# Kernel tuning notes

Hardware: AMD Instinct MI355X
Metric: run time of the kernel (lower is better)

## Reference

```python
import jax, jax.numpy as jnp
import numpy as np

NPOINT = 1024
RADIUS = 0.2
NSAMPLE = 32


def fps(xyz, npoint):
    """Furthest point sampling. xyz: (B, N, 3) -> idx (B, npoint) int32.
    Sequential farthest-distance selection, first point is index 0 (matches CUDA kernel)."""
    def one(pts):
        N = pts.shape[0]
        def step(carry, _):
            dists, last = carry
            d = jnp.sum((pts - pts[last]) ** 2, axis=-1)   # (N,)
            dists = jnp.minimum(dists, d)
            nxt = jnp.argmax(dists).astype(jnp.int32)
            return (dists, nxt), last
        init = (jnp.full((N,), 1e10, dtype=pts.dtype), jnp.int32(0))
        _, idx = jax.lax.scan(step, init, None, length=npoint)
        return idx
    return jax.vmap(one)(xyz)


def ball_query(xyz, new_xyz, radius, nsample):
    """For each centroid, indices of first nsample points within radius;
    slots with no hit are filled with the first hit (centroid itself is always a hit)."""
    N = xyz.shape[1]
    d2 = jnp.sum((new_xyz[:, :, None, :] - xyz[:, None, :, :]) ** 2, axis=-1)  # (B, npoint, N)
    cand = jnp.where(d2 < radius * radius, jnp.arange(N, dtype=jnp.int32), jnp.int32(N))
    neg_topk, _ = jax.lax.top_k(-cand, nsample)  # smallest nsample candidate indices
    idx = -neg_topk                               # ascending order, misses == N
    first = idx[..., :1]
    return jnp.where(idx == N, first, idx)


_batched_gather = jax.vmap(lambda a, i: a[i])  # a: (N, C), i: (...,) -> (..., C)


def reference(xyz, normal, features, w1, b1, w2, b2, w3, b3):
    # --- FPS sampling + gather of centroids ---
    fps_idx = fps(xyz, NPOINT)                          # (B, npoint)
    new_xyz = _batched_gather(xyz, fps_idx)             # (B, npoint, 3)
    new_normal = _batched_gather(normal, fps_idx)       # (B, npoint, 3)

    # --- ball-query grouping ---
    idx = ball_query(xyz, new_xyz, RADIUS, NSAMPLE)     # (B, npoint, nsample)
    grouped_xyz = _batched_gather(xyz, idx) - new_xyz[:, :, None, :]  # relative coords
    grouped_feat = _batched_gather(features, idx)        # (B, npoint, nsample, C)
    h = jnp.concatenate([grouped_xyz, grouped_feat], axis=-1)  # (B, npoint, nsample, 3+C)

    # --- shared per-neighborhood MLP (1x1 convs) + max pool over neighbors ---
    h = jax.nn.relu(jnp.einsum('bpsc,co->bpso', h, w1) + b1)
    h = jax.nn.relu(jnp.einsum('bpsc,co->bpso', h, w2) + b2)
    h = jax.nn.relu(jnp.einsum('bpsc,co->bpso', h, w3) + b3)
    new_features = jnp.max(h, axis=2)                   # (B, npoint, 128)
    new_features = jnp.transpose(new_features, (0, 2, 1))  # (B, 128, npoint) channel-first
    return new_xyz, new_normal, new_features


def setup_inputs() -> dict:
    key = jax.random.key(0)
    ks = jax.random.split(key, 9)
    B, N, C = 8, 8192, 32
    cin = 3 + C
    return {
        'xyz': jax.random.uniform(ks[0], (B, N, 3), dtype=jnp.float32),
        'normal': jax.random.normal(ks[1], (B, N, 3), dtype=jnp.float32),
        'features': jax.random.normal(ks[2], (B, N, C), dtype=jnp.float32),
        'w1': jax.random.normal(ks[3], (cin, 64), dtype=jnp.float32) * (1.0 / np.sqrt(cin)),
        'b1': jnp.zeros((64,), dtype=jnp.float32),
        'w2': jax.random.normal(ks[4], (64, 64), dtype=jnp.float32) * (1.0 / np.sqrt(64)),
        'b2': jnp.zeros((64,), dtype=jnp.float32),
        'w3': jax.random.normal(ks[5], (64, 128), dtype=jnp.float32) * (1.0 / np.sqrt(64)),
        'b3': jnp.zeros((128,), dtype=jnp.float32),
    }
```

## Files before the change

### kernel.cpp

```cpp
#include <hip/hip_runtime.h>

#define NB 8
#define NN 8192
#define NC 32
#define NPOINT 1024
#define NSAMPLE 32

__device__ __forceinline__ float d2_exact(float ax, float ay, float az,
                                          float bx, float by, float bz) {
    float dx = __fsub_rn(ax, bx);
    float dy = __fsub_rn(ay, by);
    float dz = __fsub_rn(az, bz);
    return __fadd_rn(__fadd_rn(__fmul_rn(dx, dx), __fmul_rn(dy, dy)),
                     __fmul_rn(dz, dz));
}

#define FPS_T 256
#define FPS_K (NN / FPS_T)

__device__ __forceinline__ unsigned long long kmax64(unsigned long long a,
                                                     unsigned long long b) {
    return a > b ? a : b;
}

template <int CTRL, int RM>
__device__ __forceinline__ unsigned long long dpp_k(unsigned long long k) {
    unsigned hi = (unsigned)__builtin_amdgcn_update_dpp(
        0, (int)(k >> 32), CTRL, RM, 0xf, true);
    unsigned lo = (unsigned)__builtin_amdgcn_update_dpp(
        0, (int)(k & 0xffffffffULL), CTRL, RM, 0xf, true);
    return ((unsigned long long)hi << 32) | lo;
}

__global__ __launch_bounds__(FPS_T, 1) void fps_kernel(
    const float* __restrict__ xyz, const float* __restrict__ normal,
    float* __restrict__ out_xyz, float* __restrict__ out_normal) {
    const int b = blockIdx.x;
    const float* bx = xyz + (size_t)b * NN * 3;
    const int tid = threadIdx.x;
    const int lane = tid & 63;
    const int wave = tid >> 6;

    __shared__ unsigned long long redk[2][4];
    __shared__ int sel_hist[NPOINT];

    float px[FPS_K], py[FPS_K], pz[FPS_K], dist[FPS_K];
#pragma unroll
    for (int k = 0; k < FPS_K; ++k) {
        int p = tid + k * FPS_T;
        px[k] = bx[p * 3 + 0];
        py[k] = bx[p * 3 + 1];
        pz[k] = bx[p * 3 + 2];
        dist[k] = 1e10f;
    }
#pragma unroll
    for (int k = 0; k < FPS_K; ++k) {
        asm volatile("" : "+v"(px[k]), "+v"(py[k]), "+v"(pz[k]));
    }

    int cur = 0;
    float lx = bx[0], ly = bx[1], lz = bx[2];

    for (int it = 0; it < NPOINT; ++it) {
        const int par = it & 1;
        if (tid == 0) sel_hist[it] = cur;

        float bv = -1.0f;
        int bk = 0;
#pragma unroll
        for (int k = 0; k < FPS_K; ++k) {
            float d = d2_exact(px[k], py[k], pz[k], lx, ly, lz);
            float nd = fminf(dist[k], d);
            dist[k] = nd;
            bool gt = nd > bv;
            bv = gt ? nd : bv;
            bk = gt ? k : bk;
        }
        int bp = tid + (bk << 8);
        unsigned long long key =
            ((unsigned long long)__float_as_uint(bv) << 32) |
            (unsigned)(~bp);

        key = kmax64(key, dpp_k<0x111, 0xf>(key));
        key = kmax64(key, dpp_k<0x112, 0xf>(key));
        key = kmax64(key, dpp_k<0x114, 0xf>(key));
        key = kmax64(key, dpp_k<0x118, 0xf>(key));
        key = kmax64(key, dpp_k<0x142, 0xa>(key));
        key = kmax64(key, dpp_k<0x143, 0xc>(key));
        if (lane == 63) redk[par][wave] = key;
        __syncthreads();

        unsigned long long g =
            kmax64(kmax64(redk[par][0], redk[par][1]),
                   kmax64(redk[par][2], redk[par][3]));
        int p = (int)(~(unsigned)(g & 0xffffffffULL));
        p = __builtin_amdgcn_readfirstlane(p);
        const float* lp = bx + 3 * (size_t)p;
        lx = lp[0]; ly = lp[1]; lz = lp[2];
        cur = p;
    }
    __syncthreads();

    const float* bn = normal + (size_t)b * NN * 3;
    for (int t = tid; t < NPOINT; t += FPS_T) {
        int i = sel_hist[t];
        size_t o = ((size_t)b * NPOINT + t) * 3;
        out_xyz[o + 0] = bx[i * 3 + 0];
        out_xyz[o + 1] = bx[i * 3 + 1];
        out_xyz[o + 2] = bx[i * 3 + 2];
        out_normal[o + 0] = bn[i * 3 + 0];
        out_normal[o + 1] = bn[i * 3 + 1];
        out_normal[o + 2] = bn[i * 3 + 2];
    }
}

#define K2_WAVES 2
#define XS 37
#define HS 65

__global__ __launch_bounds__(64 * K2_WAVES) void group_mlp_kernel(
    const float* __restrict__ xyz, const float* __restrict__ features,
    const float* __restrict__ w1, const float* __restrict__ b1,
    const float* __restrict__ w2, const float* __restrict__ b2,
    const float* __restrict__ w3, const float* __restrict__ b3,
    const float* __restrict__ new_xyz, float* __restrict__ out_feat) {
    const int wave = threadIdx.x >> 6;
    const int lane = threadIdx.x & 63;
    const int g = blockIdx.x * K2_WAVES + wave;
    const int b = g >> 10;
    const int p = g & 1023;
    const float* bxp = xyz + (size_t)b * NN * 3;
    const float* bfp = features + (size_t)b * NN * NC;

    __shared__ int sel_s[K2_WAVES][NSAMPLE];
    __shared__ float bufA[K2_WAVES][32 * HS];
    __shared__ float bufB[K2_WAVES][32 * HS];

    const float cx = new_xyz[(size_t)g * 3 + 0];
    const float cy = new_xyz[(size_t)g * 3 + 1];
    const float cz = new_xyz[(size_t)g * 3 + 2];

    int have = 0;
    for (int ch = 0; ch < NN / 64 && have < NSAMPLE; ++ch) {
        int j = ch * 64 + lane;
        float x = bxp[j * 3 + 0], y = bxp[j * 3 + 1], z = bxp[j * 3 + 2];
        float d2 = d2_exact(x, y, z, cx, cy, cz);
        bool hit = d2 < 0.04f;
        unsigned long long m = __ballot(hit);
        int pos = have + __popcll(m & ((1ull << lane) - 1ull));
        if (hit && pos < NSAMPLE) sel_s[wave][pos] = j;
        have += __popcll(m);
    }
    __syncthreads();
    int nsel = have < NSAMPLE ? have : NSAMPLE;
    int first = sel_s[wave][0];
    if (lane < NSAMPLE && lane >= nsel) sel_s[wave][lane] = first;
    __syncthreads();

    {
        int s = lane >> 1, h = lane & 1;
        int row = sel_s[wave][s];
        float* X = &bufA[wave][0];
        const float* fr = bfp + (size_t)row * NC + h * 16;
#pragma unroll
        for (int q = 0; q < 4; ++q) {
            float4 v = *(const float4*)(fr + q * 4);
            int base = s * XS + 3 + h * 16 + q * 4;
            X[base + 0] = v.x; X[base + 1] = v.y;
            X[base + 2] = v.z; X[base + 3] = v.w;
        }
        if (h == 0) {
            X[s * XS + 0] = __fsub_rn(bxp[row * 3 + 0], cx);
            X[s * XS + 1] = __fsub_rn(bxp[row * 3 + 1], cy);
            X[s * XS + 2] = __fsub_rn(bxp[row * 3 + 2], cz);
        }
    }
    __syncthreads();

    const int sg = lane >> 3;
    const int og = lane & 7;

    {
        float acc[4][8];
#pragma unroll
        for (int j = 0; j < 4; ++j)
#pragma unroll
            for (int o = 0; o < 8; ++o) acc[j][o] = 0.f;
        const float* X = &bufA[wave][0];
        for (int c = 0; c < 35; ++c) {
            float xv[4];
#pragma unroll
            for (int j = 0; j < 4; ++j) xv[j] = X[(sg * 4 + j) * XS + c];
            const float* wr = w1 + c * 64 + og * 8;
            float4 wa = *(const float4*)(wr);
            float4 wb = *(const float4*)(wr + 4);
            float w8[8] = {wa.x, wa.y, wa.z, wa.w, wb.x, wb.y, wb.z, wb.w};
#pragma unroll
            for (int j = 0; j < 4; ++j)
#pragma unroll
                for (int o = 0; o < 8; ++o) acc[j][o] += xv[j] * w8[o];
        }
        float4 ba = *(const float4*)(b1 + og * 8);
        float4 bb = *(const float4*)(b1 + og * 8 + 4);
        float bias[8] = {ba.x, ba.y, ba.z, ba.w, bb.x, bb.y, bb.z, bb.w};
        float* H = &bufB[wave][0];
#pragma unroll
        for (int j = 0; j < 4; ++j)
#pragma unroll
            for (int o = 0; o < 8; ++o)
                H[(sg * 4 + j) * HS + og * 8 + o] = fmaxf(acc[j][o] + bias[o], 0.f);
    }
    __syncthreads();

    {
        float acc[4][8];
#pragma unroll
        for (int j = 0; j < 4; ++j)
#pragma unroll
            for (int o = 0; o < 8; ++o) acc[j][o] = 0.f;
        const float* H = &bufB[wave][0];
        for (int c = 0; c < 64; ++c) {
            float xv[4];
#pragma unroll
            for (int j = 0; j < 4; ++j) xv[j] = H[(sg * 4 + j) * HS + c];
            const float* wr = w2 + c * 64 + og * 8;
            float4 wa = *(const float4*)(wr);
            float4 wb = *(const float4*)(wr + 4);
            float w8[8] = {wa.x, wa.y, wa.z, wa.w, wb.x, wb.y, wb.z, wb.w};
#pragma unroll
            for (int j = 0; j < 4; ++j)
#pragma unroll
                for (int o = 0; o < 8; ++o) acc[j][o] += xv[j] * w8[o];
        }
        float4 ba = *(const float4*)(b2 + og * 8);
        float4 bb = *(const float4*)(b2 + og * 8 + 4);
        float bias[8] = {ba.x, ba.y, ba.z, ba.w, bb.x, bb.y, bb.z, bb.w};
        float* H2 = &bufA[wave][0];
#pragma unroll
        for (int j = 0; j < 4; ++j)
#pragma unroll
            for (int o = 0; o < 8; ++o)
                H2[(sg * 4 + j) * HS + og * 8 + o] = fmaxf(acc[j][o] + bias[o], 0.f);
    }
    __syncthreads();

    {
        float acc[4][16];
#pragma unroll
        for (int j = 0; j < 4; ++j)
#pragma unroll
            for (int o = 0; o < 16; ++o) acc[j][o] = 0.f;
        const float* H = &bufA[wave][0];
        for (int c = 0; c < 64; ++c) {
            float xv[4];
#pragma unroll
            for (int j = 0; j < 4; ++j) xv[j] = H[(sg * 4 + j) * HS + c];
            const float* wr = w3 + c * 128 + og * 16;
            float4 wq[4];
#pragma unroll
            for (int q = 0; q < 4; ++q) wq[q] = *(const float4*)(wr + q * 4);
            float w16[16] = {wq[0].x, wq[0].y, wq[0].z, wq[0].w,
                             wq[1].x, wq[1].y, wq[1].z, wq[1].w,
                             wq[2].x, wq[2].y, wq[2].z, wq[2].w,
                             wq[3].x, wq[3].y, wq[3].z, wq[3].w};
#pragma unroll
            for (int j = 0; j < 4; ++j)
#pragma unroll
                for (int o = 0; o < 16; ++o) acc[j][o] += xv[j] * w16[o];
        }
        float m[16];
#pragma unroll
        for (int o = 0; o < 16; ++o) {
            float t0 = fmaxf(acc[0][o], acc[1][o]);
            float t1 = fmaxf(acc[2][o], acc[3][o]);
            m[o] = fmaxf(t0, t1);
        }
#pragma unroll
        for (int off = 8; off <= 32; off <<= 1)
#pragma unroll
            for (int o = 0; o < 16; ++o) m[o] = fmaxf(m[o], __shfl_xor(m[o], off));
        if (sg == 0) {
            float4 bq[4];
#pragma unroll
            for (int q = 0; q < 4; ++q) bq[q] = *(const float4*)(b3 + og * 16 + q * 4);
            float bias[16] = {bq[0].x, bq[0].y, bq[0].z, bq[0].w,
                              bq[1].x, bq[1].y, bq[1].z, bq[1].w,
                              bq[2].x, bq[2].y, bq[2].z, bq[2].w,
                              bq[3].x, bq[3].y, bq[3].z, bq[3].w};
#pragma unroll
            for (int o = 0; o < 16; ++o) {
                float v = fmaxf(m[o] + bias[o], 0.f);
                out_feat[((size_t)b * 128 + og * 16 + o) * NPOINT + p] = v;
            }
        }
    }
}

extern "C" void kernel_launch(void* const* d_in, const int* in_sizes, int n_in,
                              void* d_out, int out_size, void* d_ws, size_t ws_size,
                              hipStream_t stream) {
    const float* xyz      = (const float*)d_in[0];
    const float* normal   = (const float*)d_in[1];
    const float* features = (const float*)d_in[2];
    const float* w1 = (const float*)d_in[3];
    const float* b1 = (const float*)d_in[4];
    const float* w2 = (const float*)d_in[5];
    const float* b2 = (const float*)d_in[6];
    const float* w3 = (const float*)d_in[7];
    const float* b3 = (const float*)d_in[8];

    float* out        = (float*)d_out;
    float* out_xyz    = out;
    float* out_normal = out + NB * NPOINT * 3;
    float* out_feat   = out + 2 * NB * NPOINT * 3;

    hipLaunchKernelGGL(fps_kernel, dim3(NB), dim3(FPS_T), 0, stream,
                       xyz, normal, out_xyz, out_normal);
    hipLaunchKernelGGL(group_mlp_kernel, dim3(NB * NPOINT / K2_WAVES),
                       dim3(64 * K2_WAVES), 0, stream,
                       xyz, features, w1, b1, w2, b2, w3, b3, out_xyz, out_feat);
}
```

Measured before the change: 1.184 ms.

## Widen FPS block to 512 threads, use packed FP32 math and LDS-staged coordinates

Doubles the FPS block to 512 threads (eight waves) so each thread holds half as many points. The distance computation now uses packed v_pk_add/v_pk_mul pairs. The selected point's coordinates are read from a 96KB LDS copy of the cloud instead of global memory, both per iteration and in the final gather. This shortens the serial per-iteration latency of the 1024-step loop, at the cost of a wider cross-wave reduction, more waves per barrier and heavy LDS use.

```diff
diff --git a/kernel.cpp b/kernel.cpp
--- a/kernel.cpp
+++ b/kernel.cpp
@@ -15,8 +15,22 @@
                      __fmul_rn(dz, dz));
 }
 
-#define FPS_T 256
+#define FPS_T 512
 #define FPS_K (NN / FPS_T)
+#define FPS_W (FPS_T / 64)
+
+typedef float f32x2 __attribute__((ext_vector_type(2)));
+
+__device__ __forceinline__ f32x2 pk_add(f32x2 a, f32x2 b) {
+    f32x2 d;
+    asm("v_pk_add_f32 %0, %1, %2" : "=v"(d) : "v"(a), "v"(b));
+    return d;
+}
+__device__ __forceinline__ f32x2 pk_mul(f32x2 a, f32x2 b) {
+    f32x2 d;
+    asm("v_pk_mul_f32 %0, %1, %2" : "=v"(d) : "v"(a), "v"(b));
+    return d;
+}
 
 __device__ __forceinline__ unsigned long long kmax64(unsigned long long a,
                                                      unsigned long long b) {
@@ -41,21 +55,28 @@
     const int lane = tid & 63;
     const int wave = tid >> 6;
 
-    __shared__ unsigned long long redk[2][4];
+    __shared__ float sxyz[NN * 3];
+    __shared__ unsigned long long redk[2][FPS_W];
     __shared__ int sel_hist[NPOINT];
 
-    float px[FPS_K], py[FPS_K], pz[FPS_K], dist[FPS_K];
+    f32x2 px[FPS_K / 2], py[FPS_K / 2], pz[FPS_K / 2];
+    float dist[FPS_K];
 #pragma unroll
     for (int k = 0; k < FPS_K; ++k) {
         int p = tid + k * FPS_T;
-        px[k] = bx[p * 3 + 0];
-        py[k] = bx[p * 3 + 1];
-        pz[k] = bx[p * 3 + 2];
+        float x = bx[p * 3 + 0];
+        float y = bx[p * 3 + 1];
+        float z = bx[p * 3 + 2];
+        sxyz[p * 3 + 0] = x;
+        sxyz[p * 3 + 1] = y;
+        sxyz[p * 3 + 2] = z;
+        if ((k & 1) == 0) { px[k >> 1].x = x; py[k >> 1].x = y; pz[k >> 1].x = z; }
+        else              { px[k >> 1].y = x; py[k >> 1].y = y; pz[k >> 1].y = z; }
         dist[k] = 1e10f;
     }
 #pragma unroll
-    for (int k = 0; k < FPS_K; ++k) {
-        asm volatile("" : "+v"(px[k]), "+v"(py[k]), "+v"(pz[k]));
+    for (int q = 0; q < FPS_K / 2; ++q) {
+        asm volatile("" : "+v"(px[q]), "+v"(py[q]), "+v"(pz[q]));
     }
 
     int cur = 0;
@@ -65,18 +86,31 @@
         const int par = it & 1;
         if (tid == 0) sel_hist[it] = cur;
 
+        f32x2 nlx = {-lx, -lx};
+        f32x2 nly = {-ly, -ly};
+        f32x2 nlz = {-lz, -lz};
+
         float bv = -1.0f;
         int bk = 0;
 #pragma unroll
-        for (int k = 0; k < FPS_K; ++k) {
-            float d = d2_exact(px[k], py[k], pz[k], lx, ly, lz);
-            float nd = fminf(dist[k], d);
-            dist[k] = nd;
-            bool gt = nd > bv;
-            bv = gt ? nd : bv;
-            bk = gt ? k : bk;
-        }
-        int bp = tid + (bk << 8);
+        for (int q = 0; q < FPS_K / 2; ++q) {
+            f32x2 dx = pk_add(px[q], nlx);
+            f32x2 dy = pk_add(py[q], nly);
+            f32x2 dz = pk_add(pz[q], nlz);
+            f32x2 d2 = pk_add(pk_add(pk_mul(dx, dx), pk_mul(dy, dy)),
+                              pk_mul(dz, dz));
+            float nd0 = fminf(dist[2 * q + 0], d2.x);
+            float nd1 = fminf(dist[2 * q + 1], d2.y);
+            dist[2 * q + 0] = nd0;
+            dist[2 * q + 1] = nd1;
+            bool g0 = nd0 > bv;
+            bv = g0 ? nd0 : bv;
+            bk = g0 ? 2 * q + 0 : bk;
+            bool g1 = nd1 > bv;
+            bv = g1 ? nd1 : bv;
+            bk = g1 ? 2 * q + 1 : bk;
+        }
+        int bp = tid + (bk << 9);
         unsigned long long key =
             ((unsigned long long)__float_as_uint(bv) << 32) |
             (unsigned)(~bp);
@@ -91,12 +125,15 @@
         __syncthreads();
 
         unsigned long long g =
-            kmax64(kmax64(redk[par][0], redk[par][1]),
-                   kmax64(redk[par][2], redk[par][3]));
+            kmax64(kmax64(kmax64(redk[par][0], redk[par][1]),
+                          kmax64(redk[par][2], redk[par][3])),
+                   kmax64(kmax64(redk[par][4], redk[par][5]),
+                          kmax64(redk[par][6], redk[par][7])));
         int p = (int)(~(unsigned)(g & 0xffffffffULL));
         p = __builtin_amdgcn_readfirstlane(p);
-        const float* lp = bx + 3 * (size_t)p;
-        lx = lp[0]; ly = lp[1]; lz = lp[2];
+        lx = sxyz[p * 3 + 0];
+        ly = sxyz[p * 3 + 1];
+        lz = sxyz[p * 3 + 2];
         cur = p;
     }
     __syncthreads();
@@ -105,9 +142,9 @@
     for (int t = tid; t < NPOINT; t += FPS_T) {
         int i = sel_hist[t];
         size_t o = ((size_t)b * NPOINT + t) * 3;
-        out_xyz[o + 0] = bx[i * 3 + 0];
-        out_xyz[o + 1] = bx[i * 3 + 1];
-        out_xyz[o + 2] = bx[i * 3 + 2];
+        out_xyz[o + 0] = sxyz[i * 3 + 0];
+        out_xyz[o + 1] = sxyz[i * 3 + 1];
+        out_xyz[o + 2] = sxyz[i * 3 + 2];
         out_normal[o + 0] = bn[i * 3 + 0];
         out_normal[o + 1] = bn[i * 3 + 1];
         out_normal[o + 2] = bn[i * 3 + 2];
```

After: 1.334 ms. +12.6%, slower.

## Fuse FPS and grouping MLP into one persistent kernel streaming centroid indices

Applied to the files above, without the earlier changes.

Merges the FPS and group/MLP kernels into a single cooperative persistent launch. 8 blocks run FPS and publish selected indices to a workspace in chunks of 16 via atomic stores. 248 consumer blocks spin-wait on those indices and run ball query plus the MLP as soon as each centroid is ready, so the grouping work overlaps the long sequential FPS. This adds polling overhead and relies on all blocks being co-resident, with a fallback to a normal launch if the cooperative launch fails.

```diff
diff --git a/kernel.cpp b/kernel.cpp
--- a/kernel.cpp
+++ b/kernel.cpp
@@ -17,6 +17,16 @@
 
 #define FPS_T 256
 #define FPS_K (NN / FPS_T)
+#define NCONS 248
+#define NBLK (NB + NCONS)
+#define K2_WAVES 4
+#define SLOTS_PER_PASS (NCONS * K2_WAVES)
+#define NPASS ((NB * NPOINT + SLOTS_PER_PASS - 1) / SLOTS_PER_PASS)
+
+#define XS 37
+#define HS 65
+
+#define SMEM_BYTES 90112
 
 __device__ __forceinline__ unsigned long long kmax64(unsigned long long a,
                                                      unsigned long long b) {
@@ -32,268 +42,294 @@
     return ((unsigned long long)hi << 32) | lo;
 }
 
-__global__ __launch_bounds__(FPS_T, 1) void fps_kernel(
+__global__ __launch_bounds__(256, 1) void fused_kernel(
     const float* __restrict__ xyz, const float* __restrict__ normal,
-    float* __restrict__ out_xyz, float* __restrict__ out_normal) {
-    const int b = blockIdx.x;
-    const float* bx = xyz + (size_t)b * NN * 3;
-    const int tid = threadIdx.x;
-    const int lane = tid & 63;
-    const int wave = tid >> 6;
-
-    __shared__ unsigned long long redk[2][4];
-    __shared__ int sel_hist[NPOINT];
-
-    float px[FPS_K], py[FPS_K], pz[FPS_K], dist[FPS_K];
-#pragma unroll
-    for (int k = 0; k < FPS_K; ++k) {
-        int p = tid + k * FPS_T;
-        px[k] = bx[p * 3 + 0];
-        py[k] = bx[p * 3 + 1];
-        pz[k] = bx[p * 3 + 2];
-        dist[k] = 1e10f;
-    }
-#pragma unroll
-    for (int k = 0; k < FPS_K; ++k) {
-        asm volatile("" : "+v"(px[k]), "+v"(py[k]), "+v"(pz[k]));
-    }
-
-    int cur = 0;
-    float lx = bx[0], ly = bx[1], lz = bx[2];
-
-    for (int it = 0; it < NPOINT; ++it) {
-        const int par = it & 1;
-        if (tid == 0) sel_hist[it] = cur;
-
-        float bv = -1.0f;
-        int bk = 0;
-#pragma unroll
-        for (int k = 0; k < FPS_K; ++k) {
-            float d = d2_exact(px[k], py[k], pz[k], lx, ly, lz);
-            float nd = fminf(dist[k], d);
-            dist[k] = nd;
-            bool gt = nd > bv;
-            bv = gt ? nd : bv;
-            bk = gt ? k : bk;
-        }
-        int bp = tid + (bk << 8);
-        unsigned long long key =
-            ((unsigned long long)__float_as_uint(bv) << 32) |
-            (unsigned)(~bp);
-
-        key = kmax64(key, dpp_k<0x111, 0xf>(key));
-        key = kmax64(key, dpp_k<0x112, 0xf>(key));
-        key = kmax64(key, dpp_k<0x114, 0xf>(key));
-        key = kmax64(key, dpp_k<0x118, 0xf>(key));
-        key = kmax64(key, dpp_k<0x142, 0xa>(key));
-        key = kmax64(key, dpp_k<0x143, 0xc>(key));
-        if (lane == 63) redk[par][wave] = key;
-        __syncthreads();
-
-        unsigned long long g =
-            kmax64(kmax64(redk[par][0], redk[par][1]),
-                   kmax64(redk[par][2], redk[par][3]));
-        int p = (int)(~(unsigned)(g & 0xffffffffULL));
-        p = __builtin_amdgcn_readfirstlane(p);
-        const float* lp = bx + 3 * (size_t)p;
-        lx = lp[0]; ly = lp[1]; lz = lp[2];
-        cur = p;
-    }
-    __syncthreads();
-
-    const float* bn = normal + (size_t)b * NN * 3;
-    for (int t = tid; t < NPOINT; t += FPS_T) {
-        int i = sel_hist[t];
-        size_t o = ((size_t)b * NPOINT + t) * 3;
-        out_xyz[o + 0] = bx[i * 3 + 0];
-        out_xyz[o + 1] = bx[i * 3 + 1];
-        out_xyz[o + 2] = bx[i * 3 + 2];
-        out_normal[o + 0] = bn[i * 3 + 0];
-        out_normal[o + 1] = bn[i * 3 + 1];
-        out_normal[o + 2] = bn[i * 3 + 2];
-    }
-}
-
-#define K2_WAVES 2
-#define XS 37
-#define HS 65
-
-__global__ __launch_bounds__(64 * K2_WAVES) void group_mlp_kernel(
-    const float* __restrict__ xyz, const float* __restrict__ features,
+    const float* __restrict__ features,
     const float* __restrict__ w1, const float* __restrict__ b1,
     const float* __restrict__ w2, const float* __restrict__ b2,
     const float* __restrict__ w3, const float* __restrict__ b3,
-    const float* __restrict__ new_xyz, float* __restrict__ out_feat) {
-    const int wave = threadIdx.x >> 6;
-    const int lane = threadIdx.x & 63;
-    const int g = blockIdx.x * K2_WAVES + wave;
-    const int b = g >> 10;
-    const int p = g & 1023;
-    const float* bxp = xyz + (size_t)b * NN * 3;
-    const float* bfp = features + (size_t)b * NN * NC;
-
-    __shared__ int sel_s[K2_WAVES][NSAMPLE];
-    __shared__ float bufA[K2_WAVES][32 * HS];
-    __shared__ float bufB[K2_WAVES][32 * HS];
-
-    const float cx = new_xyz[(size_t)g * 3 + 0];
-    const float cy = new_xyz[(size_t)g * 3 + 1];
-    const float cz = new_xyz[(size_t)g * 3 + 2];
-
-    int have = 0;
-    for (int ch = 0; ch < NN / 64 && have < NSAMPLE; ++ch) {
-        int j = ch * 64 + lane;
-        float x = bxp[j * 3 + 0], y = bxp[j * 3 + 1], z = bxp[j * 3 + 2];
-        float d2 = d2_exact(x, y, z, cx, cy, cz);
-        bool hit = d2 < 0.04f;
-        unsigned long long m = __ballot(hit);
-        int pos = have + __popcll(m & ((1ull << lane) - 1ull));
-        if (hit && pos < NSAMPLE) sel_s[wave][pos] = j;
-        have += __popcll(m);
+    float* __restrict__ out_xyz, float* __restrict__ out_normal,
+    float* __restrict__ out_feat, int* __restrict__ idxbuf) {
+
+    __shared__ __align__(16) char smem[SMEM_BYTES];
+
+    if (blockIdx.x < NB) {
+        unsigned long long (*redk)[4] = (unsigned long long (*)[4])(smem);
+        int* sel_hist = (int*)(smem + 64);
+
+        const int b = blockIdx.x;
+        const float* bx = xyz + (size_t)b * NN * 3;
+        const int tid = threadIdx.x;
+        const int lane = tid & 63;
+        const int wave = tid >> 6;
+        int* idxg = idxbuf + (b << 10);
+
+        float px[FPS_K], py[FPS_K], pz[FPS_K], dist[FPS_K];
+#pragma unroll
+        for (int k = 0; k < FPS_K; ++k) {
+            int p = tid + k * FPS_T;
+            px[k] = bx[p * 3 + 0];
+            py[k] = bx[p * 3 + 1];
+            pz[k] = bx[p * 3 + 2];
+            dist[k] = 1e10f;
+        }
+#pragma unroll
+        for (int k = 0; k < FPS_K; ++k) {
+            asm volatile("" : "+v"(px[k]), "+v"(py[k]), "+v"(pz[k]));
+        }
+
+        int cur = 0;
+        float lx = bx[0], ly = bx[1], lz = bx[2];
+
+        for (int it = 0; it < NPOINT; ++it) {
+            const int par = it & 1;
+            if (tid == 0) sel_hist[it] = cur;
+
+            float bv = -1.0f;
+            int bk = 0;
+#pragma unroll
+            for (int k = 0; k < FPS_K; ++k) {
+                float d = d2_exact(px[k], py[k], pz[k], lx, ly, lz);
+                float nd = fminf(dist[k], d);
+                dist[k] = nd;
+                bool gt = nd > bv;
+                bv = gt ? nd : bv;
+                bk = gt ? k : bk;
+            }
+            int bp = tid + (bk << 8);
+            unsigned long long key =
+                ((unsigned long long)__float_as_uint(bv) << 32) |
+                (unsigned)(~bp);
+
+            key = kmax64(key, dpp_k<0x111, 0xf>(key));
+            key = kmax64(key, dpp_k<0x112, 0xf>(key));
+            key = kmax64(key, dpp_k<0x114, 0xf>(key));
+            key = kmax64(key, dpp_k<0x118, 0xf>(key));
+            key = kmax64(key, dpp_k<0x142, 0xa>(key));
+            key = kmax64(key, dpp_k<0x143, 0xc>(key));
+            if (lane == 63) redk[par][wave] = key;
+            __syncthreads();
+
+            unsigned long long g =
+                kmax64(kmax64(redk[par][0], redk[par][1]),
+                       kmax64(redk[par][2], redk[par][3]));
+            int p = (int)(~(unsigned)(g & 0xffffffffULL));
+            p = __builtin_amdgcn_readfirstlane(p);
+            const float* lp = bx + 3 * (size_t)p;
+            lx = lp[0]; ly = lp[1]; lz = lp[2];
+            cur = p;
+
+            if (((it & 15) == 15) && tid < 16) {
+                int t = (it & ~15) + tid;
+                __hip_atomic_store(idxg + t, sel_hist[t], __ATOMIC_RELAXED,
+                                   __HIP_MEMORY_SCOPE_AGENT);
+            }
+        }
+        __syncthreads();
+
+        const float* bn = normal + (size_t)b * NN * 3;
+        for (int t = tid; t < NPOINT; t += FPS_T) {
+            int i = sel_hist[t];
+            size_t o = ((size_t)b * NPOINT + t) * 3;
+            out_xyz[o + 0] = bx[i * 3 + 0];
+            out_xyz[o + 1] = bx[i * 3 + 1];
+            out_xyz[o + 2] = bx[i * 3 + 2];
+            out_normal[o + 0] = bn[i * 3 + 0];
+            out_normal[o + 1] = bn[i * 3 + 1];
+            out_normal[o + 2] = bn[i * 3 + 2];
+        }
+    } else {
+        int*   sel_all  = (int*)smem;
+        float* bufA_all = (float*)(smem + 512);
+        float* bufB_all = (float*)(smem + 33792);
+
+        const int cb = blockIdx.x - NB;
+        const int wave = threadIdx.x >> 6;
+        const int lane = threadIdx.x & 63;
+        int*   sel = sel_all + wave * 32;
+        float* XA  = bufA_all + wave * 2080;
+        float* XB  = bufB_all + wave * 2080;
+
+        for (int pass = 0; pass < NPASS; ++pass) {
+            int k = pass * SLOTS_PER_PASS + (cb * K2_WAVES + wave);
+            if (k >= NB * NPOINT) k -= NB * NPOINT;
+            const int b = k & 7;
+            const int t = k >> 3;
+            const int g = (b << 10) + t;
+            const int p = t;
+            const float* bxp = xyz + (size_t)b * NN * 3;
+            const float* bfp = features + (size_t)b * NN * NC;
+
+            int v = __hip_atomic_load(idxbuf + g, __ATOMIC_RELAXED,
+                                      __HIP_MEMORY_SCOPE_AGENT);
+            while (v < 0) {
+                __builtin_amdgcn_s_sleep(8);
+                v = __hip_atomic_load(idxbuf + g, __ATOMIC_RELAXED,
+                                      __HIP_MEMORY_SCOPE_AGENT);
+            }
+            const float cx = bxp[v * 3 + 0];
+            const float cy = bxp[v * 3 + 1];
+            const float cz = bxp[v * 3 + 2];
+
+            int have = 0;
+            for (int ch = 0; ch < NN / 64 && have < NSAMPLE; ++ch) {
+                int j = ch * 64 + lane;
+                float x = bxp[j * 3 + 0], y = bxp[j * 3 + 1], z = bxp[j * 3 + 2];
+                float d2 = d2_exact(x, y, z, cx, cy, cz);
+                bool hit = d2 < 0.04f;
+                unsigned long long m = __ballot(hit);
+                int pos = have + __popcll(m & ((1ull << lane) - 1ull));
+                if (hit && pos < NSAMPLE) sel[pos] = j;
+                have += __popcll(m);
+            }
+            __syncthreads();
+            int nsel = have < NSAMPLE ? have : NSAMPLE;
+            int first = sel[0];
+            if (lane < NSAMPLE && lane >= nsel) sel[lane] = first;
+            __syncthreads();
+
+            {
+                int s = lane >> 1, h = lane & 1;
+                int row = sel[s];
+                const float* fr = bfp + (size_t)row * NC + h * 16;
+#pragma unroll
+                for (int q = 0; q < 4; ++q) {
+                    float4 vv = *(const float4*)(fr + q * 4);
+                    int base = s * XS + 3 + h * 16 + q * 4;
+                    XA[base + 0] = vv.x; XA[base + 1] = vv.y;
+                    XA[base + 2] = vv.z; XA[base + 3] = vv.w;
+                }
+                if (h == 0) {
+                    XA[s * XS + 0] = __fsub_rn(bxp[row * 3 + 0], cx);
+                    XA[s * XS + 1] = __fsub_rn(bxp[row * 3 + 1], cy);
+                    XA[s * XS + 2] = __fsub_rn(bxp[row * 3 + 2], cz);
+                }
+            }
+            __syncthreads();
+
+            const int sg = lane >> 3;
+            const int og = lane & 7;
+
+            {
+                float acc[4][8];
+#pragma unroll
+                for (int j = 0; j < 4; ++j)
+#pragma unroll
+                    for (int o = 0; o < 8; ++o) acc[j][o] = 0.f;
+                for (int c = 0; c < 35; ++c) {
+                    float xv[4];
+#pragma unroll
+                    for (int j = 0; j < 4; ++j) xv[j] = XA[(sg * 4 + j) * XS + c];
+                    const float* wr = w1 + c * 64 + og * 8;
+                    float4 wa = *(const float4*)(wr);
+                    float4 wb = *(const float4*)(wr + 4);
+                    float w8[8] = {wa.x, wa.y, wa.z, wa.w, wb.x, wb.y, wb.z, wb.w};
+#pragma unroll
+                    for (int j = 0; j < 4; ++j)
+#pragma unroll
+                        for (int o = 0; o < 8; ++o) acc[j][o] += xv[j] * w8[o];
+                }
+                float4 ba = *(const float4*)(b1 + og * 8);
+                float4 bb = *(const float4*)(b1 + og * 8 + 4);
+                float bias[8] = {ba.x, ba.y, ba.z, ba.w, bb.x, bb.y, bb.z, bb.w};
+#pragma unroll
+                for (int j = 0; j < 4; ++j)
+#pragma unroll
+                    for (int o = 0; o < 8; ++o)
+                        XB[(sg * 4 + j) * HS + og * 8 + o] =
+                            fmaxf(acc[j][o] + bias[o], 0.f);
+            }
+            __syncthreads();
+
+            {
+                float acc[4][8];
+#pragma unroll
+                for (int j = 0; j < 4; ++j)
+#pragma unroll
+                    for (int o = 0; o < 8; ++o) acc[j][o] = 0.f;
+                for (int c = 0; c < 64; ++c) {
+                    float xv[4];
+#pragma unroll
+                    for (int j = 0; j < 4; ++j) xv[j] = XB[(sg * 4 + j) * HS + c];
+                    const float* wr = w2 + c * 64 + og * 8;
+                    float4 wa = *(const float4*)(wr);
+                    float4 wb = *(const float4*)(wr + 4);
+                    float w8[8] = {wa.x, wa.y, wa.z, wa.w, wb.x, wb.y, wb.z, wb.w};
+#pragma unroll
+                    for (int j = 0; j < 4; ++j)
+#pragma unroll
+                        for (int o = 0; o < 8; ++o) acc[j][o] += xv[j] * w8[o];
+                }
+                float4 ba = *(const float4*)(b2 + og * 8);
+                float4 bb = *(const float4*)(b2 + og * 8 + 4);
+                float bias[8] = {ba.x, ba.y, ba.z, ba.w, bb.x, bb.y, bb.z, bb.w};
+#pragma unroll
+                for (int j = 0; j < 4; ++j)
+#pragma unroll
+                    for (int o = 0; o < 8; ++o)
+                        XA[(sg * 4 + j) * HS + og * 8 + o] =
+                            fmaxf(acc[j][o] + bias[o], 0.f);
+            }
+            __syncthreads();
+
+            {
+                float acc[4][16];
+#pragma unroll
+                for (int j = 0; j < 4; ++j)
+#pragma unroll
+                    for (int o = 0; o < 16; ++o) acc[j][o] = 0.f;
+                for (int c = 0; c < 64; ++c) {
+                    float xv[4];
+#pragma unroll
+                    for (int j = 0; j < 4; ++j) xv[j] = XA[(sg * 4 + j) * HS + c];
+                    const float* wr = w3 + c * 128 + og * 16;
+                    float4 wq[4];
+#pragma unroll
+                    for (int q = 0; q < 4; ++q) wq[q] = *(const float4*)(wr + q * 4);
+                    float w16[16] = {wq[0].x, wq[0].y, wq[0].z, wq[0].w,
+                                     wq[1].x, wq[1].y, wq[1].z, wq[1].w,
+                                     wq[2].x, wq[2].y, wq[2].z, wq[2].w,
+                                     wq[3].x, wq[3].y, wq[3].z, wq[3].w};
+#pragma unroll
+                    for (int j = 0; j < 4; ++j)
+#pragma unroll
+                        for (int o = 0; o < 16; ++o) acc[j][o] += xv[j] * w16[o];
+                }
+                float m[16];
+#pragma unroll
+                for (int o = 0; o < 16; ++o) {
+                    float t0 = fmaxf(acc[0][o], acc[1][o]);
+                    float t1 = fmaxf(acc[2][o], acc[3][o]);
+                    m[o] = fmaxf(t0, t1);
+                }
+#pragma unroll
+                for (int off = 8; off <= 32; off <<= 1)
+#pragma unroll
+                    for (int o = 0; o < 16; ++o)
+                        m[o] = fmaxf(m[o], __shfl_xor(m[o], off));
+                if (sg == 0) {
+                    float4 bq[4];
+#pragma unroll
+                    for (int q = 0; q < 4; ++q)
+                        bq[q] = *(const float4*)(b3 + og * 16 + q * 4);
+                    float bias[16] = {bq[0].x, bq[0].y, bq[0].z, bq[0].w,
+                                      bq[1].x, bq[1].y, bq[1].z, bq[1].w,
+                                      bq[2].x, bq[2].y, bq[2].z, bq[2].w,
+                                      bq[3].x, bq[3].y, bq[3].z, bq[3].w};
+#pragma unroll
+                    for (int o = 0; o < 16; ++o) {
+                        float val = fmaxf(m[o] + bias[o], 0.f);
+                        out_feat[((size_t)b * 128 + og * 16 + o) * NPOINT + p] = val;
+                    }
+                }
+            }
+        }
     }
-    __syncthreads();
-    int nsel = have < NSAMPLE ? have : NSAMPLE;
-    int first = sel_s[wave][0];
-    if (lane < NSAMPLE && lane >= nsel) sel_s[wave][lane] = first;
-    __syncthreads();
-
-    {
-        int s = lane >> 1, h = lane & 1;
-        int row = sel_s[wave][s];
-        float* X = &bufA[wave][0];
-        const float* fr = bfp + (size_t)row * NC + h * 16;
-#pragma unroll
-        for (int q = 0; q < 4; ++q) {
-            float4 v = *(const float4*)(fr + q * 4);
-            int base = s * XS + 3 + h * 16 + q * 4;
-            X[base + 0] = v.x; X[base + 1] = v.y;
-            X[base + 2] = v.z; X[base + 3] = v.w;
-        }
-        if (h == 0) {
-            X[s * XS + 0] = __fsub_rn(bxp[row * 3 + 0], cx);
-            X[s * XS + 1] = __fsub_rn(bxp[row * 3 + 1], cy);
-            X[s * XS + 2] = __fsub_rn(bxp[row * 3 + 2], cz);
-        }
-    }
-    __syncthreads();
-
-    const int sg = lane >> 3;
-    const int og = lane & 7;
-
-    {
-        float acc[4][8];
-#pragma unroll
-        for (int j = 0; j < 4; ++j)
-#pragma unroll
-            for (int o = 0; o < 8; ++o) acc[j][o] = 0.f;
-        const float* X = &bufA[wave][0];
-        for (int c = 0; c < 35; ++c) {
-            float xv[4];
-#pragma unroll
-            for (int j = 0; j < 4; ++j) xv[j] = X[(sg * 4 + j) * XS + c];
-            const float* wr = w1 + c * 64 + og * 8;
-            float4 wa = *(const float4*)(wr);
-            float4 wb = *(const float4*)(wr + 4);
-            float w8[8] = {wa.x, wa.y, wa.z, wa.w, wb.x, wb.y, wb.z, wb.w};
-#pragma unroll
-            for (int j = 0; j < 4; ++j)
-#pragma unroll
-                for (int o = 0; o < 8; ++o) acc[j][o] += xv[j] * w8[o];
-        }
-        float4 ba = *(const float4*)(b1 + og * 8);
-        float4 bb = *(const float4*)(b1 + og * 8 + 4);
-        float bias[8] = {ba.x, ba.y, ba.z, ba.w, bb.x, bb.y, bb.z, bb.w};
-        float* H = &bufB[wave][0];
-#pragma unroll
-        for (int j = 0; j < 4; ++j)
-#pragma unroll
-            for (int o = 0; o < 8; ++o)
-                H[(sg * 4 + j) * HS + og * 8 + o] = fmaxf(acc[j][o] + bias[o], 0.f);
-    }
-    __syncthreads();
-
-    {
-        float acc[4][8];
-#pragma unroll
-        for (int j = 0; j < 4; ++j)
-#pragma unroll
-            for (int o = 0; o < 8; ++o) acc[j][o] = 0.f;
-        const float* H = &bufB[wave][0];
-        for (int c = 0; c < 64; ++c) {
-            float xv[4];
-#pragma unroll
-            for (int j = 0; j < 4; ++j) xv[j] = H[(sg * 4 + j) * HS + c];
-            const float* wr = w2 + c * 64 + og * 8;
-            float4 wa = *(const float4*)(wr);
-            float4 wb = *(const float4*)(wr + 4);
-            float w8[8] = {wa.x, wa.y, wa.z, wa.w, wb.x, wb.y, wb.z, wb.w};
-#pragma unroll
-            for (int j = 0; j < 4; ++j)
-#pragma unroll
-                for (int o = 0; o < 8; ++o) acc[j][o] += xv[j] * w8[o];
-        }
-        float4 ba = *(const float4*)(b2 + og * 8);
-        float4 bb = *(const float4*)(b2 + og * 8 + 4);
-        float bias[8] = {ba.x, ba.y, ba.z, ba.w, bb.x, bb.y, bb.z, bb.w};
-        float* H2 = &bufA[wave][0];
-#pragma unroll
-        for (int j = 0; j < 4; ++j)
-#pragma unroll
-            for (int o = 0; o < 8; ++o)
-                H2[(sg * 4 + j) * HS + og * 8 + o] = fmaxf(acc[j][o] + bias[o], 0.f);
-    }
-    __syncthreads();
-
-    {
-        float acc[4][16];
-#pragma unroll
-        for (int j = 0; j < 4; ++j)
-#pragma unroll
-            for (int o = 0; o < 16; ++o) acc[j][o] = 0.f;
-        const float* H = &bufA[wave][0];
-        for (int c = 0; c < 64; ++c) {
-            float xv[4];
-#pragma unroll
-            for (int j = 0; j < 4; ++j) xv[j] = H[(sg * 4 + j) * HS + c];
-            const float* wr = w3 + c * 128 + og * 16;
-            float4 wq[4];
-#pragma unroll
-            for (int q = 0; q < 4; ++q) wq[q] = *(const float4*)(wr + q * 4);
-            float w16[16] = {wq[0].x, wq[0].y, wq[0].z, wq[0].w,
-                             wq[1].x, wq[1].y, wq[1].z, wq[1].w,
-                             wq[2].x, wq[2].y, wq[2].z, wq[2].w,
-                             wq[3].x, wq[3].y, wq[3].z, wq[3].w};
-#pragma unroll
-            for (int j = 0; j < 4; ++j)
-#pragma unroll
-                for (int o = 0; o < 16; ++o) acc[j][o] += xv[j] * w16[o];
-        }
-        float m[16];
-#pragma unroll
-        for (int o = 0; o < 16; ++o) {
-            float t0 = fmaxf(acc[0][o], acc[1][o]);
-            float t1 = fmaxf(acc[2][o], acc[3][o]);
-            m[o] = fmaxf(t0, t1);
-        }
-#pragma unroll
-        for (int off = 8; off <= 32; off <<= 1)
-#pragma unroll
-            for (int o = 0; o < 16; ++o) m[o] = fmaxf(m[o], __shfl_xor(m[o], off));
-        if (sg == 0) {
-            float4 bq[4];
-#pragma unroll
-            for (int q = 0; q < 4; ++q) bq[q] = *(const float4*)(b3 + og * 16 + q * 4);
-            float bias[16] = {bq[0].x, bq[0].y, bq[0].z, bq[0].w,
-                              bq[1].x, bq[1].y, bq[1].z, bq[1].w,
-                              bq[2].x, bq[2].y, bq[2].z, bq[2].w,
-                              bq[3].x, bq[3].y, bq[3].z, bq[3].w};
-#pragma unroll
-            for (int o = 0; o < 16; ++o) {
-                float v = fmaxf(m[o] + bias[o], 0.f);
-                out_feat[((size_t)b * 128 + og * 16 + o) * NPOINT + p] = v;
-            }
-        }
-    }
+}
+
+__global__ void init_ws(int* __restrict__ idxbuf) {
+    int i = blockIdx.x * blockDim.x + threadIdx.x;
+    if (i < NB * NPOINT) idxbuf[i] = -1;
 }
 
 extern "C" void kernel_launch(void* const* d_in, const int* in_sizes, int n_in,
@@ -313,10 +349,21 @@
     float* out_xyz    = out;
     float* out_normal = out + NB * NPOINT * 3;
     float* out_feat   = out + 2 * NB * NPOINT * 3;
-
-    hipLaunchKernelGGL(fps_kernel, dim3(NB), dim3(FPS_T), 0, stream,
-                       xyz, normal, out_xyz, out_normal);
-    hipLaunchKernelGGL(group_mlp_kernel, dim3(NB * NPOINT / K2_WAVES),
-                       dim3(64 * K2_WAVES), 0, stream,
-                       xyz, features, w1, b1, w2, b2, w3, b3, out_xyz, out_feat);
-}
+    int*   idxbuf     = (int*)d_ws;
+
+    hipLaunchKernelGGL(init_ws, dim3(32), dim3(256), 0, stream, idxbuf);
+
+    void* args[] = {(void*)&xyz, (void*)&normal, (void*)&features,
+                    (void*)&w1, (void*)&b1, (void*)&w2, (void*)&b2,
+                    (void*)&w3, (void*)&b3,
+                    (void*)&out_xyz, (void*)&out_normal, (void*)&out_feat,
+                    (void*)&idxbuf};
+    hipError_t e = hipLaunchCooperativeKernel(
+        reinterpret_cast<void*>(fused_kernel), dim3(NBLK), dim3(256),
+        args, 0, stream);
+    if (e != hipSuccess) {
+        hipLaunchKernelGGL(fused_kernel, dim3(NBLK), dim3(256), 0, stream,
+                           xyz, normal, features, w1, b1, w2, b2, w3, b3,
+                           out_xyz, out_normal, out_feat, idxbuf);
+    }
+}
```

After: 1.039 ms. 12.2% less time.
